# Kernel optimization log

Hardware: AMD Instinct MI355X
Metric: run time of the kernel (lower is better)

## Reference

```python
import jax, jax.numpy as jnp
import numpy as np
from jax import lax

CHANNEL_N = 16
HIDDEN = 128


def _sobel_kernels(channel_n):
    dx = np.outer([1, 2, 1], [-1, 0, 1]) / 8.0  # [3,3]
    dy = dx.T
    # depthwise kernels, OIHW with I=1, O=channel_n
    wx = jnp.asarray(np.tile(dx[None, None], (channel_n, 1, 1, 1)), dtype=jnp.float32)
    wy = jnp.asarray(np.tile(dy[None, None], (channel_n, 1, 1, 1)), dtype=jnp.float32)
    return wx, wy


def _dwconv(x, w, groups):
    # x: [B,C,H,W], w: [C,1,3,3], padding=1, depthwise
    return lax.conv_general_dilated(
        x, w, window_strides=(1, 1), padding=((1, 1), (1, 1)),
        dimension_numbers=("NCHW", "OIHW", "NCHW"), feature_group_count=groups)


def _alive(x):
    # x: [B,C,H,W]; 3x3 max-pool stride 1 pad 1 on channel 3, threshold 0.1
    a = lax.reduce_window(x[:, 3:4], -jnp.inf, lax.max,
                          (1, 1, 3, 3), (1, 1, 1, 1),
                          ((0, 0), (0, 0), (1, 1), (1, 1)))
    return a > 0.1


def _update(x, W0, b0, W1, wx, wy):
    # x: [B,H,W,C] -> torch transpose(1,3) -> [B,C,W,H]
    x = jnp.swapaxes(x, 1, 3)
    B, C, Hs, Ws = x.shape
    pre = _alive(x)
    y1 = _dwconv(x, wx, C)
    y2 = _dwconv(x, wy, C)
    y = jnp.concatenate((x, y1, y2), axis=1)          # [B,3C,Hs,Ws]
    dx = jnp.swapaxes(y, 1, 3)                        # [B,Ws,Hs,3C]
    dx = jax.nn.relu(dx @ W0 + b0) @ W1               # [B,Ws,Hs,C]
    # dropout is identity in eval mode
    # faithful to torch.reshape (row-major), NOT a transpose
    dx = jnp.reshape(dx, (B, C, Hs, Hs))
    x = x + dx
    post = _alive(x)
    life = (pre & post).astype(x.dtype)
    x = x * life
    return jnp.swapaxes(x, 1, 3)


def reference(x, W0, b0, W1, steps):
    wx, wy = _sobel_kernels(CHANNEL_N)
    for _ in range(steps):
        x = _update(x, W0, b0, W1, wx, wy)
    return x


def setup_inputs() -> dict:
    key = jax.random.key(0)
    k1, k2, k3, k4 = jax.random.split(key, 4)
    B, H, W, C = 32, 128, 128, CHANNEL_N
    x = jax.random.uniform(k1, (B, H, W, C), dtype=jnp.float32)
    W0 = jax.random.normal(k2, (3 * C, HIDDEN), dtype=jnp.float32) * 0.1
    b0 = jax.random.normal(k3, (HIDDEN,), dtype=jnp.float32) * 0.01
    W1 = jax.random.normal(k4, (HIDDEN, C), dtype=jnp.float32) * 0.1
    return {"x": x, "W0": W0, "b0": b0, "W1": W1, "steps": 8}
```

## Files before the change

kernel.cpp:

```cpp
#include <hip/hip_runtime.h>

typedef _Float16 h8 __attribute__((ext_vector_type(8)));
typedef __fp16 fp16x2 __attribute__((ext_vector_type(2)));
typedef float f4 __attribute__((ext_vector_type(4)));
typedef unsigned int u32;

#define HW 128
#define PLANE (HW*HW*16)
#define NPIX (32*HW*HW)

static __device__ __forceinline__ void split2(float a, float b, u32& hi, u32& lo) {
  fp16x2 h = __builtin_amdgcn_cvt_pkrtz(a, b);
  fp16x2 l = __builtin_amdgcn_cvt_pkrtz(a - (float)h[0], b - (float)h[1]);
  union { fp16x2 v; u32 w; } uh, ul; uh.v = h; ul.v = l;
  hi = uh.w; lo = ul.w;
}

__global__ __launch_bounds__(256) void k_wprep(const float* __restrict__ W0,
    const float* __restrict__ W1, const float* __restrict__ b0,
    _Float16* __restrict__ W0Fh, _Float16* __restrict__ W0Fl,
    _Float16* __restrict__ W1Fh, _Float16* __restrict__ W1Fl) {
  int tid = threadIdx.x;
  for (int i = tid; i < 8192; i += 256) {
    int j = i & 7, lane = (i >> 3) & 63, nf = (i >> 9) & 7, kf = i >> 12;
    int gg = lane >> 4, k = kf * 32 + gg * 8 + j, n = nf * 16 + (lane & 15);
    float v = (k < 48) ? W0[k * 128 + n] : ((k == 63) ? b0[n] : 0.f);
    _Float16 hi = (_Float16)v;
    W0Fh[i] = hi; W0Fl[i] = (_Float16)(v - (float)hi);
  }
  for (int i = tid; i < 2048; i += 256) {
    int j = i & 7, lane = (i >> 3) & 63, kf = i >> 9;
    int gg = lane >> 4, k = kf * 32 + gg * 8 + j, c = lane & 15;
    float v = W1[k * 16 + c];
    _Float16 hi = (_Float16)v;
    W1Fh[i] = hi; W1Fl[i] = (_Float16)(v - (float)hi);
  }
}

#define LDQ(cc, q) do {                                              \
    int _cc = (cc);                                                  \
    bool vc = ((unsigned)_cc < 128u);                                \
    const f4* p0 = (const f4*)(rp0 + _cc * 16);                      \
    const f4* p1 = (const f4*)(rp1 + _cc * 16);                      \
    const f4* p2 = (const f4*)(rp2 + _cc * 16);                      \
    bool b0_ = vc && vh0, b2_ = vc && vh2;                           \
    q[0][0] = b0_ ? p0[0] : zero4;  q[0][1] = b0_ ? p0[1] : zero4;   \
    q[1][0] = vc  ? p1[0] : zero4;  q[1][1] = vc  ? p1[1] : zero4;   \
    q[2][0] = b2_ ? p2[0] : zero4;  q[2][1] = b2_ ? p2[1] : zero4;   \
  } while (0)

#define PROCQ(q, S) do {                                             \
    c_r1[S][0] = q[1][0];  c_r1[S][1] = q[1][1];                     \
    c_d[S][0]  = q[2][0] - q[0][0];                                  \
    c_d[S][1]  = q[2][1] - q[0][1];                                  \
    c_v[S][0]  = q[0][0] + 2.f * q[1][0] + q[2][0];                  \
    c_v[S][1]  = q[0][1] + 2.f * q[1][1] + q[2][1];                  \
  } while (0)

__global__ __launch_bounds__(256, 2) void k_mlp(const float* __restrict__ x,
    float* __restrict__ dxp, const _Float16* __restrict__ W0Fh,
    const _Float16* __restrict__ W0Fl, const _Float16* __restrict__ W1Fh,
    const _Float16* __restrict__ W1Fl) {
  __shared__ __align__(16) char smem[57344];
  const int tid = threadIdx.x;
  const int lane = tid & 63, wv = tid >> 6;
  const int g = lane >> 4, m = lane & 15;
  const int b = blockIdx.x >> 4, cd = blockIdx.x & 15;
  const float* xb = x + (size_t)b * PLANE;
  float* dpl = dxp + (size_t)(b * 16 + cd) * (HW * HW);

  {
    float4* dst = (float4*)smem;
    const float4* src = (const float4*)W0Fl;
    for (int i = tid; i < 1536; i += 256) dst[i] = src[i];
  }
  __syncthreads();

  h8 w0h[2][8];
  #pragma unroll
  for (int kf = 0; kf < 2; ++kf)
    #pragma unroll
    for (int nf = 0; nf < 8; ++nf)
      w0h[kf][nf] = *(const h8*)(W0Fh + ((kf * 8 + nf) * 64 + lane) * 8);

  const f4 zero4 = {0.f, 0.f, 0.f, 0.f};
  const int ch0 = (g & 1) * 8;
  const bool lowg = (g < 2);
  char* Hb = smem + 24576 + wv * 8192 + m * 512;
  const int mx = (m & 7) << 4;

  for (int rr = 0; rr < 2; ++rr) {
    const int hp = cd * 8 + wv * 2 + rr;
    const bool vh0 = hp >= 1, vh2 = hp <= 126;
    const float* rp0 = xb + ((size_t)(hp - 1) * 128) * 16 + ch0;
    const float* rp1 = xb + ((size_t)hp * 128) * 16 + ch0;
    const float* rp2 = xb + ((size_t)(hp + 1) * 128) * 16 + ch0;
    float* dbase = dpl + (size_t)(hp & 7) * 16 + m + (size_t)g * 4 * 128;

    f4 c_r1[3][2], c_d[3][2], c_v[3][2];
    {
      f4 q[3][2];
      LDQ(8 * m - 1, q); PROCQ(q, 0);
      LDQ(8 * m,     q); PROCQ(q, 1);
      LDQ(8 * m + 1, q); PROCQ(q, 2);
    }

    #pragma unroll
    for (int u = 0; u < 8; ++u) {
      f4 nq[3][2];
      if (u < 7) LDQ(8 * m + u + 2, nq);

      f4 cen0 = c_r1[1][0], cen1 = c_r1[1][1];
      f4 sH0 = (c_d[0][0] + 2.f * c_d[1][0] + c_d[2][0]) * 0.125f;
      f4 sH1 = (c_d[0][1] + 2.f * c_d[1][1] + c_d[2][1]) * 0.125f;
      f4 sW0 = (c_v[2][0] - c_v[0][0]) * 0.125f;
      f4 sW1 = (c_v[2][1] - c_v[0][1]) * 0.125f;

      f4 f0lo = lowg ? cen0 : sH0, f0hi = lowg ? cen1 : sH1;
      f4 f1lo = lowg ? sW0 : zero4, f1hi = lowg ? sW1 : zero4;

      union { h8 v; u32 u[4]; } b0h, b0l, b1h, b1l;
      #pragma unroll
      for (int q = 0; q < 4; ++q) {
        float a0 = (q < 2) ? f0lo[2 * q]     : f0hi[2 * q - 4];
        float a1 = (q < 2) ? f0lo[2 * q + 1] : f0hi[2 * q - 3];
        split2(a0, a1, b0h.u[q], b0l.u[q]);
        float c0 = (q < 2) ? f1lo[2 * q]     : f1hi[2 * q - 4];
        float c1 = (q < 2) ? f1lo[2 * q + 1] : f1hi[2 * q - 3];
        split2(c0, c1, b1h.u[q], b1l.u[q]);
      }
      if (g == 3) {
        b1h.u[3] = (b1h.u[3] & 0xFFFFu) | 0x3C000000u;
        b1l.u[3] =  b1l.u[3] & 0xFFFFu;
      }
      f4 acc[8];
      #pragma unroll
      for (int nf = 0; nf < 8; ++nf) acc[nf] = zero4;
      #pragma unroll
      for (int nf = 0; nf < 8; ++nf) {
        h8 l0 = *(const h8*)(smem + (0 * 8 + nf) * 1024 + lane * 16);
        h8 l1 = *(const h8*)(smem + (1 * 8 + nf) * 1024 + lane * 16);
        acc[nf] = __builtin_amdgcn_mfma_f32_16x16x32_f16(w0h[0][nf], b0h.v, acc[nf], 0, 0, 0);
        acc[nf] = __builtin_amdgcn_mfma_f32_16x16x32_f16(w0h[1][nf], b1h.v, acc[nf], 0, 0, 0);
        acc[nf] = __builtin_amdgcn_mfma_f32_16x16x32_f16(w0h[0][nf], b0l.v, acc[nf], 0, 0, 0);
        acc[nf] = __builtin_amdgcn_mfma_f32_16x16x32_f16(w0h[1][nf], b1l.v, acc[nf], 0, 0, 0);
        acc[nf] = __builtin_amdgcn_mfma_f32_16x16x32_f16(l0, b0h.v, acc[nf], 0, 0, 0);
        acc[nf] = __builtin_amdgcn_mfma_f32_16x16x32_f16(l1, b1h.v, acc[nf], 0, 0, 0);
      }
      #pragma unroll
      for (int nf = 0; nf < 8; ++nf) {
        float r0 = fmaxf(acc[nf][0], 0.f), r1 = fmaxf(acc[nf][1], 0.f);
        float r2 = fmaxf(acc[nf][2], 0.f), r3 = fmaxf(acc[nf][3], 0.f);
        uint2 ph, pl;
        split2(r0, r1, ph.x, pl.x);
        split2(r2, r3, ph.y, pl.y);
        int off = (nf * 32 + g * 8) ^ mx;
        *(uint2*)(Hb + off) = ph;
        *(uint2*)(Hb + 256 + off) = pl;
      }
      asm volatile("" ::: "memory");
      __builtin_amdgcn_s_waitcnt(0xC07F);
      f4 acc2 = zero4;
      #pragma unroll
      for (int kf = 0; kf < 4; ++kf) {
        h8 w1h = *(const h8*)(smem + 16384 + kf * 1024 + lane * 16);
        h8 w1l = *(const h8*)(smem + 20480 + kf * 1024 + lane * 16);
        int hoff = (kf * 64 + g * 16) ^ mx;
        h8 hh = *(const h8*)(Hb + hoff);
        h8 hl = *(const h8*)(Hb + 256 + hoff);
        acc2 = __builtin_amdgcn_mfma_f32_16x16x32_f16(w1h, hh, acc2, 0, 0, 0);
        acc2 = __builtin_amdgcn_mfma_f32_16x16x32_f16(w1h, hl, acc2, 0, 0, 0);
        acc2 = __builtin_amdgcn_mfma_f32_16x16x32_f16(w1l, hh, acc2, 0, 0, 0);
      }
      #pragma unroll
      for (int r = 0; r < 4; ++r)
        dbase[(size_t)(u * 16 + r) * 128] = acc2[r];

      if (u < 7) {
        #pragma unroll
        for (int j = 0; j < 2; ++j) {
          c_r1[0][j] = c_r1[1][j]; c_d[0][j] = c_d[1][j]; c_v[0][j] = c_v[1][j];
          c_r1[1][j] = c_r1[2][j]; c_d[1][j] = c_d[2][j]; c_v[1][j] = c_v[2][j];
        }
        PROCQ(nq, 2);
      }
    }
  }
}

__global__ __launch_bounds__(256) void k_addlife(const float* __restrict__ xo,
    const float* __restrict__ dxp, float* __restrict__ xn) {
  int p = blockIdx.x * 256 + threadIdx.x;
  int b = p >> 14, rem = p & 16383;
  int h = rem >> 7, w = rem & 127;
  const float* xop = xo + (size_t)p * 16;
  const float* dplane = dxp + (size_t)b * 16 * 16384;
  f4 xv[4];
  #pragma unroll
  for (int i = 0; i < 4; ++i) xv[i] = *(const f4*)(xop + i * 4);
  float dxv[16];
  #pragma unroll
  for (int c = 0; c < 16; ++c) dxv[c] = dplane[c * 16384 + rem];
  f4 nv[4];
  #pragma unroll
  for (int i = 0; i < 4; ++i) {
    nv[i][0] = xv[i][0] + dxv[i * 4 + 0];
    nv[i][1] = xv[i][1] + dxv[i * 4 + 1];
    nv[i][2] = xv[i][2] + dxv[i * 4 + 2];
    nv[i][3] = xv[i][3] + dxv[i * 4 + 3];
  }
  float pre = -1e30f, post = -1e30f;
  const float* xb3 = xo + (size_t)b * 16384 * 16 + 3;
  const float* d3p = dplane + 3 * 16384;
  #pragma unroll
  for (int dh = -1; dh <= 1; ++dh)
    #pragma unroll
    for (int dw = -1; dw <= 1; ++dw) {
      int hh = h + dh, ww = w + dw;
      bool v = ((unsigned)hh < 128u) && ((unsigned)ww < 128u);
      int rp = hh * 128 + ww;
      float x3 = v ? xb3[(size_t)rp * 16] : -1e30f;
      float d3 = v ? d3p[rp] : 0.f;
      pre = fmaxf(pre, x3);
      post = fmaxf(post, v ? (x3 + d3) : -1e30f);
    }
  bool life = (pre > 0.1f) && (post > 0.1f);
  float* out = xn + (size_t)p * 16;
  f4 z = {0.f, 0.f, 0.f, 0.f};
  #pragma unroll
  for (int i = 0; i < 4; ++i) *(f4*)(out + i * 4) = life ? nv[i] : z;
}

extern "C" void kernel_launch(void* const* d_in, const int* in_sizes, int n_in,
                              void* d_out, int out_size, void* d_ws, size_t ws_size,
                              hipStream_t stream) {
  const float* x0 = (const float*)d_in[0];
  const float* W0 = (const float*)d_in[1];
  const float* b0 = (const float*)d_in[2];
  const float* W1 = (const float*)d_in[3];

  float*    A    = (float*)d_ws;
  float*    dxp  = (float*)((char*)d_ws + ((size_t)32 << 20));
  _Float16* W0Fh = (_Float16*)((char*)d_ws + ((size_t)64 << 20));
  _Float16* W0Fl = W0Fh + 8192;
  _Float16* W1Fh = W0Fl + 8192;
  _Float16* W1Fl = W1Fh + 2048;
  float*    Bo   = (float*)d_out;

  k_wprep<<<1, 256, 0, stream>>>(W0, W1, b0, W0Fh, W0Fl, W1Fh, W1Fl);

  const float* xcur = x0;
  for (int s = 1; s <= 8; ++s) {
    k_mlp<<<512, 256, 0, stream>>>(xcur, dxp, W0Fh, W0Fl, W1Fh, W1Fl);
    float* xnext = (s & 1) ? A : Bo;
    k_addlife<<<2048, 256, 0, stream>>>(xcur, dxp, xnext);
    xcur = xnext;
  }
}
```

Before: 581.4 us.

## Feed hidden activations to second MFMA directly from registers, dropping LDS staging

Reorders the second-layer weight fragment layout in the prep kernel so that the output of two first-layer 16x16 MFMA tiles maps straight onto the B operand of the second-layer MFMA. The hidden activations no longer go through shared memory, which removes the LDS writes, the wait and the LDS reads for the hidden buffer, and shrinks shared memory from 56 KB to 24 KB. The smaller footprint may allow more resident blocks. The second layer now interleaves with the first in four chunks and uses two accumulators to shorten dependency chains, at the cost of a different accumulation order.

```diff
diff --git a/kernel.cpp b/kernel.cpp
--- a/kernel.cpp
+++ b/kernel.cpp
@@ -30,7 +30,8 @@
   }
   for (int i = tid; i < 2048; i += 256) {
     int j = i & 7, lane = (i >> 3) & 63, kf = i >> 9;
-    int gg = lane >> 4, k = kf * 32 + gg * 8 + j, c = lane & 15;
+    int gg = lane >> 4, c = lane & 15;
+    int k = kf * 32 + ((j >> 2) << 4) + gg * 4 + (j & 3);
     float v = W1[k * 16 + c];
     _Float16 hi = (_Float16)v;
     W1Fh[i] = hi; W1Fl[i] = (_Float16)(v - (float)hi);
@@ -61,7 +62,7 @@
     float* __restrict__ dxp, const _Float16* __restrict__ W0Fh,
     const _Float16* __restrict__ W0Fl, const _Float16* __restrict__ W1Fh,
     const _Float16* __restrict__ W1Fl) {
-  __shared__ __align__(16) char smem[57344];
+  __shared__ __align__(16) char smem[24576];
   const int tid = threadIdx.x;
   const int lane = tid & 63, wv = tid >> 6;
   const int g = lane >> 4, m = lane & 15;
@@ -86,8 +87,6 @@
   const f4 zero4 = {0.f, 0.f, 0.f, 0.f};
   const int ch0 = (g & 1) * 8;
   const bool lowg = (g < 2);
-  char* Hb = smem + 24576 + wv * 8192 + m * 512;
-  const int mx = (m & 7) << 4;
 
   for (int rr = 0; rr < 2; ++rr) {
     const int hp = cd * 8 + wv * 2 + rr;
@@ -133,45 +132,46 @@
         b1h.u[3] = (b1h.u[3] & 0xFFFFu) | 0x3C000000u;
         b1l.u[3] =  b1l.u[3] & 0xFFFFu;
       }
-      f4 acc[8];
+
+      f4 acc2a = zero4, acc2b = zero4;
       #pragma unroll
-      for (int nf = 0; nf < 8; ++nf) acc[nf] = zero4;
-      #pragma unroll
-      for (int nf = 0; nf < 8; ++nf) {
-        h8 l0 = *(const h8*)(smem + (0 * 8 + nf) * 1024 + lane * 16);
-        h8 l1 = *(const h8*)(smem + (1 * 8 + nf) * 1024 + lane * 16);
-        acc[nf] = __builtin_amdgcn_mfma_f32_16x16x32_f16(w0h[0][nf], b0h.v, acc[nf], 0, 0, 0);
-        acc[nf] = __builtin_amdgcn_mfma_f32_16x16x32_f16(w0h[1][nf], b1h.v, acc[nf], 0, 0, 0);
-        acc[nf] = __builtin_amdgcn_mfma_f32_16x16x32_f16(w0h[0][nf], b0l.v, acc[nf], 0, 0, 0);
-        acc[nf] = __builtin_amdgcn_mfma_f32_16x16x32_f16(w0h[1][nf], b1l.v, acc[nf], 0, 0, 0);
-        acc[nf] = __builtin_amdgcn_mfma_f32_16x16x32_f16(l0, b0h.v, acc[nf], 0, 0, 0);
-        acc[nf] = __builtin_amdgcn_mfma_f32_16x16x32_f16(l1, b1h.v, acc[nf], 0, 0, 0);
-      }
-      #pragma unroll
-      for (int nf = 0; nf < 8; ++nf) {
-        float r0 = fmaxf(acc[nf][0], 0.f), r1 = fmaxf(acc[nf][1], 0.f);
-        float r2 = fmaxf(acc[nf][2], 0.f), r3 = fmaxf(acc[nf][3], 0.f);
-        uint2 ph, pl;
-        split2(r0, r1, ph.x, pl.x);
-        split2(r2, r3, ph.y, pl.y);
-        int off = (nf * 32 + g * 8) ^ mx;
-        *(uint2*)(Hb + off) = ph;
-        *(uint2*)(Hb + 256 + off) = pl;
-      }
-      asm volatile("" ::: "memory");
-      __builtin_amdgcn_s_waitcnt(0xC07F);
-      f4 acc2 = zero4;
-      #pragma unroll
-      for (int kf = 0; kf < 4; ++kf) {
-        h8 w1h = *(const h8*)(smem + 16384 + kf * 1024 + lane * 16);
-        h8 w1l = *(const h8*)(smem + 20480 + kf * 1024 + lane * 16);
-        int hoff = (kf * 64 + g * 16) ^ mx;
-        h8 hh = *(const h8*)(Hb + hoff);
-        h8 hl = *(const h8*)(Hb + 256 + hoff);
-        acc2 = __builtin_amdgcn_mfma_f32_16x16x32_f16(w1h, hh, acc2, 0, 0, 0);
-        acc2 = __builtin_amdgcn_mfma_f32_16x16x32_f16(w1h, hl, acc2, 0, 0, 0);
-        acc2 = __builtin_amdgcn_mfma_f32_16x16x32_f16(w1l, hh, acc2, 0, 0, 0);
-      }
+      for (int p = 0; p < 4; ++p) {
+        f4 aA = zero4, aB = zero4;
+        {
+          const int nf = 2 * p;
+          h8 l0 = *(const h8*)(smem + nf * 1024 + lane * 16);
+          h8 l1 = *(const h8*)(smem + 8192 + nf * 1024 + lane * 16);
+          aA = __builtin_amdgcn_mfma_f32_16x16x32_f16(w0h[0][nf], b0h.v, aA, 0, 0, 0);
+          aA = __builtin_amdgcn_mfma_f32_16x16x32_f16(w0h[1][nf], b1h.v, aA, 0, 0, 0);
+          aA = __builtin_amdgcn_mfma_f32_16x16x32_f16(w0h[0][nf], b0l.v, aA, 0, 0, 0);
+          aA = __builtin_amdgcn_mfma_f32_16x16x32_f16(w0h[1][nf], b1l.v, aA, 0, 0, 0);
+          aA = __builtin_amdgcn_mfma_f32_16x16x32_f16(l0, b0h.v, aA, 0, 0, 0);
+          aA = __builtin_amdgcn_mfma_f32_16x16x32_f16(l1, b1h.v, aA, 0, 0, 0);
+        }
+        {
+          const int nf = 2 * p + 1;
+          h8 l0 = *(const h8*)(smem + nf * 1024 + lane * 16);
+          h8 l1 = *(const h8*)(smem + 8192 + nf * 1024 + lane * 16);
+          aB = __builtin_amdgcn_mfma_f32_16x16x32_f16(w0h[0][nf], b0h.v, aB, 0, 0, 0);
+          aB = __builtin_amdgcn_mfma_f32_16x16x32_f16(w0h[1][nf], b1h.v, aB, 0, 0, 0);
+          aB = __builtin_amdgcn_mfma_f32_16x16x32_f16(w0h[0][nf], b0l.v, aB, 0, 0, 0);
+          aB = __builtin_amdgcn_mfma_f32_16x16x32_f16(w0h[1][nf], b1l.v, aB, 0, 0, 0);
+          aB = __builtin_amdgcn_mfma_f32_16x16x32_f16(l0, b0h.v, aB, 0, 0, 0);
+          aB = __builtin_amdgcn_mfma_f32_16x16x32_f16(l1, b1h.v, aB, 0, 0, 0);
+        }
+        union { h8 v; u32 u[4]; } hh, hl;
+        split2(fmaxf(aA[0], 0.f), fmaxf(aA[1], 0.f), hh.u[0], hl.u[0]);
+        split2(fmaxf(aA[2], 0.f), fmaxf(aA[3], 0.f), hh.u[1], hl.u[1]);
+        split2(fmaxf(aB[0], 0.f), fmaxf(aB[1], 0.f), hh.u[2], hl.u[2]);
+        split2(fmaxf(aB[2], 0.f), fmaxf(aB[3], 0.f), hh.u[3], hl.u[3]);
+        h8 w1hp = *(const h8*)(smem + 16384 + p * 1024 + lane * 16);
+        h8 w1lp = *(const h8*)(smem + 20480 + p * 1024 + lane * 16);
+        acc2a = __builtin_amdgcn_mfma_f32_16x16x32_f16(w1hp, hh.v, acc2a, 0, 0, 0);
+        acc2b = __builtin_amdgcn_mfma_f32_16x16x32_f16(w1hp, hl.v, acc2b, 0, 0, 0);
+        acc2a = __builtin_amdgcn_mfma_f32_16x16x32_f16(w1lp, hh.v, acc2a, 0, 0, 0);
+      }
+      f4 acc2 = acc2a + acc2b;
+
       #pragma unroll
       for (int r = 0; r < 4; ++r)
         dbase[(size_t)(u * 16 + r) * 128] = acc2[r];
```

Measured after the change: 938.6 us. +61.4%, slower.
